# Kernel tuning notes

Measured on AMD Instinct MI355X. Metric: run time of the kernel, lower is better.

## Reference

```python
import jax, jax.numpy as jnp
import numpy as np

DEPTH = 6
N_LEAF = 2 ** DEPTH          # 64
GATE_COUNT = N_LEAF - 1      # 63
IN_F = 512
OUT_F = 512
BATCH = 1024


def setup_inputs() -> dict:
    key = jax.random.key(0)
    k1, k2, k3 = jax.random.split(key, 3)
    x = jax.random.normal(k1, (BATCH, IN_F), dtype=jnp.float32)
    gw = jax.random.normal(k2, (IN_F, GATE_COUNT), dtype=jnp.float32)
    gb = jnp.zeros((GATE_COUNT,), dtype=jnp.float32)
    pw = jax.random.normal(k3, (OUT_F, IN_F, N_LEAF), dtype=jnp.float32)
    pb = jnp.zeros((OUT_F, N_LEAF), dtype=jnp.float32)
    return {"x": x, "gw": gw, "gb": gb, "pw": pw, "pb": pb}


def _leaf_probs(x, gw, gb, depth):
    # gatings: sigmoid(x @ gw + gb), shape [B, gate_count]
    g = jax.nn.sigmoid(x @ gw + gb)
    B = x.shape[0]
    dens = jnp.ones((B, 1), dtype=x.dtype)  # root density
    offset = 0
    for d in range(depth):
        n = 2 ** d
        gp = g[:, offset:offset + n]                    # parent gatings [B, n]
        # left child multiplies by g, right child by (1 - g), interleaved
        pair = jnp.stack([gp, 1.0 - gp], axis=-1).reshape(B, 2 * n)
        dens = jnp.repeat(dens, 2, axis=1) * pair        # [B, 2n]
        offset += n
    return dens  # [B, n_leaf]


def reference(x, gw, gb, pw, pb):
    leaf = _leaf_probs(x, gw, gb, DEPTH)                 # [B, L]
    # per-leaf linear projections, then mix with leaf probabilities
    y = jnp.einsum('bi,oil->bol', x, pw)                 # [B, O, L]
    out = jnp.einsum('bol,bl->bo', y, leaf) + leaf @ pb.T
    return out
```

## Files before the change

### kernel.cpp

```cpp
#include <hip/hip_runtime.h>
#include <hip/hip_bf16.h>

#define TDEPTH 6
#define NLEAF 64
#define NGATE 63
#define INF 512
#define OUTF 512
#define BATCH 1024

#define BM 128
#define BN 64
#define SPLITK 16
#define KCH 513
#define THREADS 256
#define XPITCH 36
#define BPITCH 144

typedef __attribute__((ext_vector_type(4)))  float f32x4;
typedef __attribute__((ext_vector_type(16))) float f32x16;
typedef __attribute__((ext_vector_type(8)))  __bf16 bf16x8;

__global__ __launch_bounds__(256) void leaf_kernel(
    const float* __restrict__ x, const float* __restrict__ gw,
    const float* __restrict__ gb, float* __restrict__ leaf) {
  const int wid = threadIdx.x >> 6, lane = threadIdx.x & 63;
  const int b = blockIdx.x * 4 + wid;
  __shared__ float g[4][NLEAF];
  if (lane < NGATE) {
    const float* xr = x + (size_t)b * INF;
    float a0 = 0.f, a1 = 0.f, a2 = 0.f, a3 = 0.f;
    #pragma unroll 4
    for (int i = 0; i < INF; i += 4) {
      a0 += xr[i + 0] * gw[(i + 0) * NGATE + lane];
      a1 += xr[i + 1] * gw[(i + 1) * NGATE + lane];
      a2 += xr[i + 2] * gw[(i + 2) * NGATE + lane];
      a3 += xr[i + 3] * gw[(i + 3) * NGATE + lane];
    }
    float t = (a0 + a1) + (a2 + a3) + gb[lane];
    g[wid][lane] = 1.0f / (1.0f + __expf(-t));
  }
  __syncthreads();
  float p = 1.0f;
  #pragma unroll
  for (int d = 0; d < TDEPTH; d++) {
    int prefix = lane >> (TDEPTH - 1 - d);
    int node = (1 << d) - 1 + (prefix >> 1);
    float gv = g[wid][node];
    p *= (prefix & 1) ? (1.0f - gv) : gv;
  }
  leaf[(size_t)b * NLEAF + lane] = p;
}

__device__ __forceinline__ void sync_raw() {
  asm volatile("s_waitcnt lgkmcnt(0)" ::: "memory");
  __builtin_amdgcn_sched_barrier(0);
  __builtin_amdgcn_s_barrier();
  __builtin_amdgcn_sched_barrier(0);
}

__global__ __launch_bounds__(THREADS, 4) void gemm_kernel(
    const float* __restrict__ x, const float* __restrict__ pw,
    const float* __restrict__ pb, const float* __restrict__ leaf,
    float* __restrict__ partial) {
  __shared__ __align__(16) float xsm[BM * XPITCH];
  __shared__ __align__(16) __bf16 Bsm[2][BN * (BPITCH/2)];

  const int tid = threadIdx.x;
  const int lane = tid & 63;
  const int wid = tid >> 6;
  const int lo = lane & 31;
  const int half = lane >> 5;

  const int bid = blockIdx.x;
  const int nb = bid & 7, mb = (bid >> 3) & 7, s = bid >> 6;
  const int m0 = mb * BM, n0 = nb * BN;
  const int cs = (s * KCH) / SPLITK;
  const int ce = ((s + 1) * KCH) / SPLITK;
  const int nreal = min(ce, INF) - cs;
  const int total = nreal + ((ce == KCH) ? 1 : 0);

  const int xrow = wid * 32 + lo;

  f32x4 lf[4][2];
  {
    const float* lr = leaf + (size_t)(m0 + xrow) * NLEAF + half * 8;
    #pragma unroll
    for (int t4 = 0; t4 < 4; t4++) {
      lf[t4][0] = *(const f32x4*)(lr + t4 * 16);
      lf[t4][1] = *(const f32x4*)(lr + t4 * 16 + 4);
    }
  }

  {
    int r = tid >> 1, h = tid & 1;
    const float* src = x + (size_t)(m0 + r) * INF + cs + h * 16;
    float* dst = xsm + r * XPITCH + h * 16;
    #pragma unroll
    for (int j = 0; j < 4; j++)
      *(f32x4*)(dst + j * 4) = *(const f32x4*)(src + j * 4);
  }

  const int bo = tid >> 2, bc = tid & 3;
  const float* pwrow = pw + (size_t)(n0 + bo) * (INF * NLEAF) + bc * 16;
  const float* pbrow = pb + (size_t)(n0 + bo) * NLEAF + bc * 16;

  f32x16 acc0 = (f32x16)(0.f), acc1 = (f32x16)(0.f);

  f32x4 bv[4];
  {
    const float* sp = pwrow + (size_t)cs * NLEAF;
    #pragma unroll
    for (int j = 0; j < 4; j++) bv[j] = *(const f32x4*)(sp + j * 4);
    #pragma unroll
    for (int h = 0; h < 2; h++) {
      f32x4 a = bv[2 * h], b = bv[2 * h + 1];
      bf16x8 w;
      w[0] = (__bf16)a[0]; w[1] = (__bf16)a[1];
      w[2] = (__bf16)a[2]; w[3] = (__bf16)a[3];
      w[4] = (__bf16)b[0]; w[5] = (__bf16)b[1];
      w[6] = (__bf16)b[2]; w[7] = (__bf16)b[3];
      *(bf16x8*)((char*)&Bsm[0][0] + bo * BPITCH + bc * 32 + h * 16) = w;
    }
  }
  sync_raw();

  __bf16* cur = &Bsm[0][0];
  __bf16* nxt = &Bsm[1][0];
  for (int t = 0; t < total; ++t) {
    const bool more = (t + 1 < total);
    if (more) {
      const float* sp = (t + 1 < nreal)
          ? pwrow + (size_t)(cs + t + 1) * NLEAF : pbrow;
      #pragma unroll
      for (int j = 0; j < 4; j++) bv[j] = *(const f32x4*)(sp + j * 4);
    }
    float xvr = xsm[xrow * XPITCH + (t & 31)];
    float xv = (t < nreal) ? xvr : 1.0f;
    bf16x8 afr[4];
    #pragma unroll
    for (int t4 = 0; t4 < 4; t4++) {
      f32x4 p0 = lf[t4][0] * xv, p1 = lf[t4][1] * xv;
      bf16x8 a;
      a[0] = (__bf16)p0[0]; a[1] = (__bf16)p0[1];
      a[2] = (__bf16)p0[2]; a[3] = (__bf16)p0[3];
      a[4] = (__bf16)p1[0]; a[5] = (__bf16)p1[1];
      a[6] = (__bf16)p1[2]; a[7] = (__bf16)p1[3];
      afr[t4] = a;
    }
    #pragma unroll
    for (int t4 = 0; t4 < 4; t4++) {
      bf16x8 b0 = *(const bf16x8*)((const char*)cur + lo * BPITCH +
                                   t4 * 32 + half * 16);
      bf16x8 b1 = *(const bf16x8*)((const char*)cur + (32 + lo) * BPITCH +
                                   t4 * 32 + half * 16);
      acc0 = __builtin_amdgcn_mfma_f32_32x32x16_bf16(afr[t4], b0, acc0, 0, 0, 0);
      acc1 = __builtin_amdgcn_mfma_f32_32x32x16_bf16(afr[t4], b1, acc1, 0, 0, 0);
    }
    if (more) {
      #pragma unroll
      for (int h = 0; h < 2; h++) {
        f32x4 a = bv[2 * h], b = bv[2 * h + 1];
        bf16x8 w;
        w[0] = (__bf16)a[0]; w[1] = (__bf16)a[1];
        w[2] = (__bf16)a[2]; w[3] = (__bf16)a[3];
        w[4] = (__bf16)b[0]; w[5] = (__bf16)b[1];
        w[6] = (__bf16)b[2]; w[7] = (__bf16)b[3];
        *(bf16x8*)((char*)nxt + bo * BPITCH + bc * 32 + h * 16) = w;
      }
    }
    sync_raw();
    __bf16* tmp = cur; cur = nxt; nxt = tmp;
  }

  float* dst = partial + ((size_t)s * BATCH + m0 + wid * 32) * OUTF + n0;
  #pragma unroll
  for (int e = 0; e < 16; e++) {
    int row = (e & 3) + 8 * (e >> 2) + 4 * half;
    dst[(size_t)row * OUTF + lo] = acc0[e];
    dst[(size_t)row * OUTF + 32 + lo] = acc1[e];
  }
}

__global__ __launch_bounds__(256) void reduce_kernel(
    const float* __restrict__ partial, float* __restrict__ out) {
  size_t e = ((size_t)blockIdx.x * 256 + threadIdx.x) * 4;
  f32x4 sum = (f32x4){0.f, 0.f, 0.f, 0.f};
  #pragma unroll
  for (int s = 0; s < SPLITK; s++)
    sum += *(const f32x4*)(partial + (size_t)s * BATCH * OUTF + e);
  *(f32x4*)(out + e) = sum;
}

extern "C" void kernel_launch(void* const* d_in, const int* in_sizes, int n_in,
                              void* d_out, int out_size, void* d_ws, size_t ws_size,
                              hipStream_t stream) {
  const float* x  = (const float*)d_in[0];
  const float* gw = (const float*)d_in[1];
  const float* gb = (const float*)d_in[2];
  const float* pw = (const float*)d_in[3];
  const float* pb = (const float*)d_in[4];
  float* out = (float*)d_out;

  float* leaf    = (float*)d_ws;
  float* partial = (float*)((char*)d_ws + (1 << 19));

  leaf_kernel<<<BATCH / 4, 256, 0, stream>>>(x, gw, gb, leaf);
  gemm_kernel<<<(BATCH / BM) * (OUTF / BN) * SPLITK, THREADS, 0, stream>>>(
      x, pw, pb, leaf, partial);
  reduce_kernel<<<(BATCH * OUTF) / (256 * 4), 256, 0, stream>>>(partial, out);
}
```

Before: 74.38 us.

## Load fp32 weights directly into LDS with swizzle and double M tile

The GEMM now stages raw fp32 pw rows into XOR-swizzled LDS using global_load_lds, rather than loading to registers and converting to bf16 before the LDS store. Each wave computes a 64x64 tile with four accumulators (BM raised to 256), so each loaded weight tile serves twice as many rows. Split-K becomes a template parameter, using 32 splits when workspace allows, with a block-index remap to group blocks that share weights. The intent is to cut register-staging overhead and raise weight reuse. In exchange it uses more LDS for fp32 tiles, converts to bf16 on the read side, and writes twice as much partial-sum data for the reduce kernel to read.

```diff
diff --git a/kernel.cpp b/kernel.cpp
--- a/kernel.cpp
+++ b/kernel.cpp
@@ -8,13 +8,10 @@
 #define OUTF 512
 #define BATCH 1024
 
-#define BM 128
+#define BM 256
 #define BN 64
-#define SPLITK 16
+#define THREADS 256
 #define KCH 513
-#define THREADS 256
-#define XPITCH 36
-#define BPITCH 144
 
 typedef __attribute__((ext_vector_type(4)))  float f32x4;
 typedef __attribute__((ext_vector_type(16))) float f32x16;
@@ -51,142 +48,198 @@
   leaf[(size_t)b * NLEAF + lane] = p;
 }
 
-__device__ __forceinline__ void sync_raw() {
-  asm volatile("s_waitcnt lgkmcnt(0)" ::: "memory");
+__device__ __forceinline__ void gload_lds16(const void* g, void* l) {
+  __builtin_amdgcn_global_load_lds(
+      (const __attribute__((address_space(1))) void*)g,
+      (__attribute__((address_space(3))) void*)l, 16, 0, 0);
+}
+
+__device__ __forceinline__ void sync_step() {
   __builtin_amdgcn_sched_barrier(0);
+  asm volatile("s_waitcnt vmcnt(0) lgkmcnt(0)" ::: "memory");
   __builtin_amdgcn_s_barrier();
   __builtin_amdgcn_sched_barrier(0);
 }
 
-__global__ __launch_bounds__(THREADS, 4) void gemm_kernel(
+template <int S>
+__global__ __launch_bounds__(THREADS, 3) void gemm_kernel(
     const float* __restrict__ x, const float* __restrict__ pw,
     const float* __restrict__ pb, const float* __restrict__ leaf,
     float* __restrict__ partial) {
-  __shared__ __align__(16) float xsm[BM * XPITCH];
-  __shared__ __align__(16) __bf16 Bsm[2][BN * (BPITCH/2)];
-
-  const int tid = threadIdx.x;
-  const int lane = tid & 63;
-  const int wid = tid >> 6;
-  const int lo = lane & 31;
-  const int half = lane >> 5;
-
-  const int bid = blockIdx.x;
-  const int nb = bid & 7, mb = (bid >> 3) & 7, s = bid >> 6;
+  constexpr int XN = KCH / S;
+  __shared__ __align__(16) unsigned char Bsm[2][BN * 256];
+  __shared__ __align__(16) float xsm[XN * BM];
+
+  const int tid = threadIdx.x, lane = tid & 63, w = tid >> 6;
+  const int lo = lane & 31, half = lane >> 5;
+
+  constexpr int NWG = 4 * 8 * S;
+  const int L = (blockIdx.x & 7) * (NWG / 8) + (blockIdx.x >> 3);
+  const int mb = L & 3;
+  const int pair = L >> 2;
+  const int nb = pair & 7, s = pair >> 3;
   const int m0 = mb * BM, n0 = nb * BN;
-  const int cs = (s * KCH) / SPLITK;
-  const int ce = ((s + 1) * KCH) / SPLITK;
-  const int nreal = min(ce, INF) - cs;
-  const int total = nreal + ((ce == KCH) ? 1 : 0);
-
-  const int xrow = wid * 32 + lo;
-
-  f32x4 lf[4][2];
+  const int cs = XN * s;
+  const bool bias = (s == S - 1);
+
+  const int lq = lane >> 4;
+  const unsigned cb = (unsigned)(lane & 15) * 16;
+  unsigned pwoff[4];
+  #pragma unroll
+  for (int j = 0; j < 4; j++) {
+    int r = w * 16 + j * 4 + lq;
+    pwoff[j] = (unsigned)(n0 + r) * (unsigned)(INF * NLEAF * 4) +
+               (cb ^ ((unsigned)(r & 7) << 4));
+  }
+  const char* pwc = (const char*)pw;
+  const char* pbc = (const char*)pb;
+
   {
-    const float* lr = leaf + (size_t)(m0 + xrow) * NLEAF + half * 8;
+    const float* src = x + (size_t)(m0 + tid) * INF + cs;
+    float v[XN];
+    #pragma unroll
+    for (int c = 0; c < XN; c += 4) {
+      f32x4 t4v = *(const f32x4*)(src + c);
+      v[c] = t4v[0]; v[c + 1] = t4v[1]; v[c + 2] = t4v[2]; v[c + 3] = t4v[3];
+    }
+    #pragma unroll
+    for (int c = 0; c < XN; c++) xsm[c * BM + tid] = v[c];
+  }
+
+  f32x4 lf[2][4][2];
+  #pragma unroll
+  for (int mr = 0; mr < 2; mr++) {
+    const float* lr = leaf + (size_t)(m0 + w * 64 + mr * 32 + lo) * NLEAF + half * 8;
     #pragma unroll
     for (int t4 = 0; t4 < 4; t4++) {
-      lf[t4][0] = *(const f32x4*)(lr + t4 * 16);
-      lf[t4][1] = *(const f32x4*)(lr + t4 * 16 + 4);
-    }
-  }
-
-  {
-    int r = tid >> 1, h = tid & 1;
-    const float* src = x + (size_t)(m0 + r) * INF + cs + h * 16;
-    float* dst = xsm + r * XPITCH + h * 16;
-    #pragma unroll
-    for (int j = 0; j < 4; j++)
-      *(f32x4*)(dst + j * 4) = *(const f32x4*)(src + j * 4);
-  }
-
-  const int bo = tid >> 2, bc = tid & 3;
-  const float* pwrow = pw + (size_t)(n0 + bo) * (INF * NLEAF) + bc * 16;
-  const float* pbrow = pb + (size_t)(n0 + bo) * NLEAF + bc * 16;
-
-  f32x16 acc0 = (f32x16)(0.f), acc1 = (f32x16)(0.f);
-
-  f32x4 bv[4];
-  {
-    const float* sp = pwrow + (size_t)cs * NLEAF;
-    #pragma unroll
-    for (int j = 0; j < 4; j++) bv[j] = *(const f32x4*)(sp + j * 4);
-    #pragma unroll
-    for (int h = 0; h < 2; h++) {
-      f32x4 a = bv[2 * h], b = bv[2 * h + 1];
-      bf16x8 w;
-      w[0] = (__bf16)a[0]; w[1] = (__bf16)a[1];
-      w[2] = (__bf16)a[2]; w[3] = (__bf16)a[3];
-      w[4] = (__bf16)b[0]; w[5] = (__bf16)b[1];
-      w[6] = (__bf16)b[2]; w[7] = (__bf16)b[3];
-      *(bf16x8*)((char*)&Bsm[0][0] + bo * BPITCH + bc * 32 + h * 16) = w;
-    }
-  }
-  sync_raw();
-
-  __bf16* cur = &Bsm[0][0];
-  __bf16* nxt = &Bsm[1][0];
-  for (int t = 0; t < total; ++t) {
-    const bool more = (t + 1 < total);
-    if (more) {
-      const float* sp = (t + 1 < nreal)
-          ? pwrow + (size_t)(cs + t + 1) * NLEAF : pbrow;
+      lf[mr][t4][0] = *(const f32x4*)(lr + t4 * 16);
+      lf[mr][t4][1] = *(const f32x4*)(lr + t4 * 16 + 4);
+    }
+  }
+
+  auto stage = [&](int buf, int t) {
+    const int i = cs + t;
+    char* dstb = (char*)&Bsm[buf][0] + w * 4096;
+    if (i < INF) {
+      const char* srcb = pwc + (size_t)i * 256;
       #pragma unroll
-      for (int j = 0; j < 4; j++) bv[j] = *(const f32x4*)(sp + j * 4);
-    }
-    float xvr = xsm[xrow * XPITCH + (t & 31)];
-    float xv = (t < nreal) ? xvr : 1.0f;
-    bf16x8 afr[4];
+      for (int j = 0; j < 4; j++) gload_lds16(srcb + pwoff[j], dstb + j * 1024);
+    } else {
+      #pragma unroll
+      for (int j = 0; j < 4; j++) {
+        int r = w * 16 + j * 4 + lq;
+        unsigned o = (unsigned)(n0 + r) * (unsigned)(NLEAF * 4) +
+                     (cb ^ ((unsigned)(r & 7) << 4));
+        gload_lds16(pbc + o, dstb + j * 1024);
+      }
+    }
+  };
+
+  f32x16 acc00 = (f32x16)(0.f), acc01 = (f32x16)(0.f);
+  f32x16 acc10 = (f32x16)(0.f), acc11 = (f32x16)(0.f);
+
+  const unsigned swz = (unsigned)(lo & 7) << 4;
+
+  stage(0, 0);
+  sync_step();
+
+  #pragma unroll 2
+  for (int t = 0; t < XN; t++) {
+    const int cur = t & 1;
+    if (t + 1 < XN || bias) stage(cur ^ 1, t + 1);
+
+    const float xv0 = xsm[t * BM + w * 64 + lo];
+    const float xv1 = xsm[t * BM + w * 64 + 32 + lo];
+    const unsigned char* bufc = &Bsm[cur][0];
+
     #pragma unroll
     for (int t4 = 0; t4 < 4; t4++) {
-      f32x4 p0 = lf[t4][0] * xv, p1 = lf[t4][1] * xv;
-      bf16x8 a;
-      a[0] = (__bf16)p0[0]; a[1] = (__bf16)p0[1];
-      a[2] = (__bf16)p0[2]; a[3] = (__bf16)p0[3];
-      a[4] = (__bf16)p1[0]; a[5] = (__bf16)p1[1];
-      a[6] = (__bf16)p1[2]; a[7] = (__bf16)p1[3];
-      afr[t4] = a;
-    }
+      const unsigned kb = (unsigned)(t4 * 64 + half * 32);
+      f32x4 b0a = *(const f32x4*)(bufc + lo * 256 + ((kb) ^ swz));
+      f32x4 b0b = *(const f32x4*)(bufc + lo * 256 + ((kb + 16) ^ swz));
+      f32x4 b1a = *(const f32x4*)(bufc + (32 + lo) * 256 + ((kb) ^ swz));
+      f32x4 b1b = *(const f32x4*)(bufc + (32 + lo) * 256 + ((kb + 16) ^ swz));
+      bf16x8 bf0, bf1;
+      bf0[0] = (__bf16)b0a[0]; bf0[1] = (__bf16)b0a[1];
+      bf0[2] = (__bf16)b0a[2]; bf0[3] = (__bf16)b0a[3];
+      bf0[4] = (__bf16)b0b[0]; bf0[5] = (__bf16)b0b[1];
+      bf0[6] = (__bf16)b0b[2]; bf0[7] = (__bf16)b0b[3];
+      bf1[0] = (__bf16)b1a[0]; bf1[1] = (__bf16)b1a[1];
+      bf1[2] = (__bf16)b1a[2]; bf1[3] = (__bf16)b1a[3];
+      bf1[4] = (__bf16)b1b[0]; bf1[5] = (__bf16)b1b[1];
+      bf1[6] = (__bf16)b1b[2]; bf1[7] = (__bf16)b1b[3];
+
+      f32x4 p0a = lf[0][t4][0] * xv0, p0b = lf[0][t4][1] * xv0;
+      f32x4 p1a = lf[1][t4][0] * xv1, p1b = lf[1][t4][1] * xv1;
+      bf16x8 a0, a1;
+      a0[0] = (__bf16)p0a[0]; a0[1] = (__bf16)p0a[1];
+      a0[2] = (__bf16)p0a[2]; a0[3] = (__bf16)p0a[3];
+      a0[4] = (__bf16)p0b[0]; a0[5] = (__bf16)p0b[1];
+      a0[6] = (__bf16)p0b[2]; a0[7] = (__bf16)p0b[3];
+      a1[0] = (__bf16)p1a[0]; a1[1] = (__bf16)p1a[1];
+      a1[2] = (__bf16)p1a[2]; a1[3] = (__bf16)p1a[3];
+      a1[4] = (__bf16)p1b[0]; a1[5] = (__bf16)p1b[1];
+      a1[6] = (__bf16)p1b[2]; a1[7] = (__bf16)p1b[3];
+
+      acc00 = __builtin_amdgcn_mfma_f32_32x32x16_bf16(a0, bf0, acc00, 0, 0, 0);
+      acc01 = __builtin_amdgcn_mfma_f32_32x32x16_bf16(a0, bf1, acc01, 0, 0, 0);
+      acc10 = __builtin_amdgcn_mfma_f32_32x32x16_bf16(a1, bf0, acc10, 0, 0, 0);
+      acc11 = __builtin_amdgcn_mfma_f32_32x32x16_bf16(a1, bf1, acc11, 0, 0, 0);
+    }
+    sync_step();
+  }
+
+  if (bias) {
+    const unsigned char* bufc = &Bsm[XN & 1][0];
     #pragma unroll
     for (int t4 = 0; t4 < 4; t4++) {
-      bf16x8 b0 = *(const bf16x8*)((const char*)cur + lo * BPITCH +
-                                   t4 * 32 + half * 16);
-      bf16x8 b1 = *(const bf16x8*)((const char*)cur + (32 + lo) * BPITCH +
-                                   t4 * 32 + half * 16);
-      acc0 = __builtin_amdgcn_mfma_f32_32x32x16_bf16(afr[t4], b0, acc0, 0, 0, 0);
-      acc1 = __builtin_amdgcn_mfma_f32_32x32x16_bf16(afr[t4], b1, acc1, 0, 0, 0);
-    }
-    if (more) {
-      #pragma unroll
-      for (int h = 0; h < 2; h++) {
-        f32x4 a = bv[2 * h], b = bv[2 * h + 1];
-        bf16x8 w;
-        w[0] = (__bf16)a[0]; w[1] = (__bf16)a[1];
-        w[2] = (__bf16)a[2]; w[3] = (__bf16)a[3];
-        w[4] = (__bf16)b[0]; w[5] = (__bf16)b[1];
-        w[6] = (__bf16)b[2]; w[7] = (__bf16)b[3];
-        *(bf16x8*)((char*)nxt + bo * BPITCH + bc * 32 + h * 16) = w;
-      }
-    }
-    sync_raw();
-    __bf16* tmp = cur; cur = nxt; nxt = tmp;
-  }
-
-  float* dst = partial + ((size_t)s * BATCH + m0 + wid * 32) * OUTF + n0;
+      const unsigned kb = (unsigned)(t4 * 64 + half * 32);
+      f32x4 b0a = *(const f32x4*)(bufc + lo * 256 + ((kb) ^ swz));
+      f32x4 b0b = *(const f32x4*)(bufc + lo * 256 + ((kb + 16) ^ swz));
+      f32x4 b1a = *(const f32x4*)(bufc + (32 + lo) * 256 + ((kb) ^ swz));
+      f32x4 b1b = *(const f32x4*)(bufc + (32 + lo) * 256 + ((kb + 16) ^ swz));
+      bf16x8 bf0, bf1, a0, a1;
+      bf0[0] = (__bf16)b0a[0]; bf0[1] = (__bf16)b0a[1];
+      bf0[2] = (__bf16)b0a[2]; bf0[3] = (__bf16)b0a[3];
+      bf0[4] = (__bf16)b0b[0]; bf0[5] = (__bf16)b0b[1];
+      bf0[6] = (__bf16)b0b[2]; bf0[7] = (__bf16)b0b[3];
+      bf1[0] = (__bf16)b1a[0]; bf1[1] = (__bf16)b1a[1];
+      bf1[2] = (__bf16)b1a[2]; bf1[3] = (__bf16)b1a[3];
+      bf1[4] = (__bf16)b1b[0]; bf1[5] = (__bf16)b1b[1];
+      bf1[6] = (__bf16)b1b[2]; bf1[7] = (__bf16)b1b[3];
+      a0[0] = (__bf16)lf[0][t4][0][0]; a0[1] = (__bf16)lf[0][t4][0][1];
+      a0[2] = (__bf16)lf[0][t4][0][2]; a0[3] = (__bf16)lf[0][t4][0][3];
+      a0[4] = (__bf16)lf[0][t4][1][0]; a0[5] = (__bf16)lf[0][t4][1][1];
+      a0[6] = (__bf16)lf[0][t4][1][2]; a0[7] = (__bf16)lf[0][t4][1][3];
+      a1[0] = (__bf16)lf[1][t4][0][0]; a1[1] = (__bf16)lf[1][t4][0][1];
+      a1[2] = (__bf16)lf[1][t4][0][2]; a1[3] = (__bf16)lf[1][t4][0][3];
+      a1[4] = (__bf16)lf[1][t4][1][0]; a1[5] = (__bf16)lf[1][t4][1][1];
+      a1[6] = (__bf16)lf[1][t4][1][2]; a1[7] = (__bf16)lf[1][t4][1][3];
+      acc00 = __builtin_amdgcn_mfma_f32_32x32x16_bf16(a0, bf0, acc00, 0, 0, 0);
+      acc01 = __builtin_amdgcn_mfma_f32_32x32x16_bf16(a0, bf1, acc01, 0, 0, 0);
+      acc10 = __builtin_amdgcn_mfma_f32_32x32x16_bf16(a1, bf0, acc10, 0, 0, 0);
+      acc11 = __builtin_amdgcn_mfma_f32_32x32x16_bf16(a1, bf1, acc11, 0, 0, 0);
+    }
+  }
+
+  float* dst = partial + ((size_t)s * BATCH + m0 + w * 64) * OUTF + n0;
   #pragma unroll
   for (int e = 0; e < 16; e++) {
     int row = (e & 3) + 8 * (e >> 2) + 4 * half;
-    dst[(size_t)row * OUTF + lo] = acc0[e];
-    dst[(size_t)row * OUTF + 32 + lo] = acc1[e];
-  }
-}
-
+    dst[(size_t)row * OUTF + lo] = acc00[e];
+    dst[(size_t)row * OUTF + 32 + lo] = acc01[e];
+    dst[(size_t)(row + 32) * OUTF + lo] = acc10[e];
+    dst[(size_t)(row + 32) * OUTF + 32 + lo] = acc11[e];
+  }
+}
+
+template <int S>
 __global__ __launch_bounds__(256) void reduce_kernel(
     const float* __restrict__ partial, float* __restrict__ out) {
   size_t e = ((size_t)blockIdx.x * 256 + threadIdx.x) * 4;
   f32x4 sum = (f32x4){0.f, 0.f, 0.f, 0.f};
   #pragma unroll
-  for (int s = 0; s < SPLITK; s++)
+  for (int s = 0; s < S; s++)
     sum += *(const f32x4*)(partial + (size_t)s * BATCH * OUTF + e);
   *(f32x4*)(out + e) = sum;
 }
@@ -202,10 +255,16 @@
   float* out = (float*)d_out;
 
   float* leaf    = (float*)d_ws;
-  float* partial = (float*)((char*)d_ws + (1 << 19));
+  float* partial = (float*)((char*)d_ws + (1 << 20));
 
   leaf_kernel<<<BATCH / 4, 256, 0, stream>>>(x, gw, gb, leaf);
-  gemm_kernel<<<(BATCH / BM) * (OUTF / BN) * SPLITK, THREADS, 0, stream>>>(
-      x, pw, pb, leaf, partial);
-  reduce_kernel<<<(BATCH * OUTF) / (256 * 4), 256, 0, stream>>>(partial, out);
-}
+
+  const size_t need32 = (size_t)(1 << 20) + (size_t)32 * BATCH * OUTF * 4;
+  if (ws_size >= need32) {
+    gemm_kernel<32><<<4 * 8 * 32, THREADS, 0, stream>>>(x, pw, pb, leaf, partial);
+    reduce_kernel<32><<<(BATCH * OUTF) / (256 * 4), 256, 0, stream>>>(partial, out);
+  } else {
+    gemm_kernel<16><<<4 * 8 * 16, THREADS, 0, stream>>>(x, pw, pb, leaf, partial);
+    reduce_kernel<16><<<(BATCH * OUTF) / (256 * 4), 256, 0, stream>>>(partial, out);
+  }
+}
```

Result: slower. 108.8 us (+46.2%).

## Pre-convert weights to bf16 MFMA-fragment layout and use single-wave register-fed GEMM blocks

Applied to the files above, without the earlier changes.

A prep kernel, fused with the leaf-probability computation, converts pw and pb to bf16 once per call and stores them in a layout that matches the MFMA B-fragments. The GEMM kernel then reads those fragments straight from global memory into registers with double buffering, which removes the shared-memory staging and the block barriers. Each wave now computes a 128x32 tile with four accumulators, so one B fragment serves four row subtiles. This adds an extra full pass over pw (read fp32, write bf16, read bf16 again) in exchange for cheaper, barrier-free GEMM loops with more reuse per fragment.

```diff
diff --git a/kernel.cpp b/kernel.cpp
--- a/kernel.cpp
+++ b/kernel.cpp
@@ -7,177 +7,167 @@
 #define INF 512
 #define OUTF 512
 #define BATCH 1024
-
-#define BM 128
-#define BN 64
 #define SPLITK 16
-#define KCH 513
-#define THREADS 256
-#define XPITCH 36
-#define BPITCH 144
 
 typedef __attribute__((ext_vector_type(4)))  float f32x4;
 typedef __attribute__((ext_vector_type(16))) float f32x16;
 typedef __attribute__((ext_vector_type(8)))  __bf16 bf16x8;
 
-__global__ __launch_bounds__(256) void leaf_kernel(
+__device__ __forceinline__ bf16x8 pack8(f32x4 a, f32x4 b) {
+  bf16x8 w;
+  w[0] = (__bf16)a[0]; w[1] = (__bf16)a[1];
+  w[2] = (__bf16)a[2]; w[3] = (__bf16)a[3];
+  w[4] = (__bf16)b[0]; w[5] = (__bf16)b[1];
+  w[6] = (__bf16)b[2]; w[7] = (__bf16)b[3];
+  return w;
+}
+
+__global__ __launch_bounds__(256) void prep_kernel(
     const float* __restrict__ x, const float* __restrict__ gw,
-    const float* __restrict__ gb, float* __restrict__ leaf) {
-  const int wid = threadIdx.x >> 6, lane = threadIdx.x & 63;
-  const int b = blockIdx.x * 4 + wid;
-  __shared__ float g[4][NLEAF];
-  if (lane < NGATE) {
-    const float* xr = x + (size_t)b * INF;
-    float a0 = 0.f, a1 = 0.f, a2 = 0.f, a3 = 0.f;
-    #pragma unroll 4
-    for (int i = 0; i < INF; i += 4) {
-      a0 += xr[i + 0] * gw[(i + 0) * NGATE + lane];
-      a1 += xr[i + 1] * gw[(i + 1) * NGATE + lane];
-      a2 += xr[i + 2] * gw[(i + 2) * NGATE + lane];
-      a3 += xr[i + 3] * gw[(i + 3) * NGATE + lane];
-    }
-    float t = (a0 + a1) + (a2 + a3) + gb[lane];
-    g[wid][lane] = 1.0f / (1.0f + __expf(-t));
-  }
-  __syncthreads();
-  float p = 1.0f;
-  #pragma unroll
-  for (int d = 0; d < TDEPTH; d++) {
-    int prefix = lane >> (TDEPTH - 1 - d);
-    int node = (1 << d) - 1 + (prefix >> 1);
-    float gv = g[wid][node];
-    p *= (prefix & 1) ? (1.0f - gv) : gv;
-  }
-  leaf[(size_t)b * NLEAF + lane] = p;
-}
-
-__device__ __forceinline__ void sync_raw() {
-  asm volatile("s_waitcnt lgkmcnt(0)" ::: "memory");
-  __builtin_amdgcn_sched_barrier(0);
-  __builtin_amdgcn_s_barrier();
-  __builtin_amdgcn_sched_barrier(0);
-}
-
-__global__ __launch_bounds__(THREADS, 4) void gemm_kernel(
-    const float* __restrict__ x, const float* __restrict__ pw,
-    const float* __restrict__ pb, const float* __restrict__ leaf,
-    float* __restrict__ partial) {
-  __shared__ __align__(16) float xsm[BM * XPITCH];
-  __shared__ __align__(16) __bf16 Bsm[2][BN * (BPITCH/2)];
-
+    const float* __restrict__ gb, const float* __restrict__ pw,
+    const float* __restrict__ pb, float* __restrict__ leaf,
+    __bf16* __restrict__ pwb) {
   const int tid = threadIdx.x;
-  const int lane = tid & 63;
-  const int wid = tid >> 6;
-  const int lo = lane & 31;
-  const int half = lane >> 5;
-
-  const int bid = blockIdx.x;
-  const int nb = bid & 7, mb = (bid >> 3) & 7, s = bid >> 6;
-  const int m0 = mb * BM, n0 = nb * BN;
-  const int cs = (s * KCH) / SPLITK;
-  const int ce = ((s + 1) * KCH) / SPLITK;
-  const int nreal = min(ce, INF) - cs;
-  const int total = nreal + ((ce == KCH) ? 1 : 0);
-
-  const int xrow = wid * 32 + lo;
-
-  f32x4 lf[4][2];
-  {
-    const float* lr = leaf + (size_t)(m0 + xrow) * NLEAF + half * 8;
+  if (blockIdx.x < 256) {
+    const int wid = tid >> 6, lane = tid & 63;
+    const int b = blockIdx.x * 4 + wid;
+    __shared__ float g[4][NLEAF];
+    if (lane < NGATE) {
+      const float* xr = x + (size_t)b * INF;
+      float a0 = 0.f, a1 = 0.f, a2 = 0.f, a3 = 0.f;
+      #pragma unroll 4
+      for (int i = 0; i < INF; i += 4) {
+        a0 += xr[i + 0] * gw[(i + 0) * NGATE + lane];
+        a1 += xr[i + 1] * gw[(i + 1) * NGATE + lane];
+        a2 += xr[i + 2] * gw[(i + 2) * NGATE + lane];
+        a3 += xr[i + 3] * gw[(i + 3) * NGATE + lane];
+      }
+      float t = (a0 + a1) + (a2 + a3) + gb[lane];
+      g[wid][lane] = 1.0f / (1.0f + __expf(-t));
+    }
+    __syncthreads();
+    float p = 1.0f;
+    #pragma unroll
+    for (int d = 0; d < TDEPTH; d++) {
+      int prefix = lane >> (TDEPTH - 1 - d);
+      int node = (1 << d) - 1 + (prefix >> 1);
+      float gv = g[wid][node];
+      p *= (prefix & 1) ? (1.0f - gv) : gv;
+    }
+    leaf[(size_t)b * NLEAF + lane] = p;
+    return;
+  }
+  const int bid2 = blockIdx.x - 256;
+  const int w = tid >> 6, lane = tid & 63;
+  const int lo = lane & 31, half = lane >> 5;
+  #pragma unroll
+  for (int it = 0; it < 8; it++) {
+    const unsigned S = (unsigned)bid2 * 32 + w * 8 + it;
+    const unsigned i_lin = S >> 2, kc = S & 3;
+    const unsigned nb32 = i_lin / 513;
+    const unsigned i = i_lin - nb32 * 513;
+    const unsigned o = nb32 * 32 + lo;
+    const unsigned l = kc * 16 + half * 8;
+    const float* src = (i < INF) ? (pw + ((size_t)o * INF + i) * NLEAF + l)
+                                 : (pb + (size_t)o * NLEAF + l);
+    f32x4 a = *(const f32x4*)src;
+    f32x4 b = *(const f32x4*)(src + 4);
+    *(bf16x8*)((char*)pwb + (size_t)S * 1024 + (size_t)lane * 16) = pack8(a, b);
+  }
+}
+
+__global__ __launch_bounds__(64, 2) void gemm_kernel(
+    const __bf16* __restrict__ pwb, const float* __restrict__ x,
+    const float* __restrict__ leaf, float* __restrict__ partial) {
+  __shared__ __align__(16) float xsm[32][128];
+
+  const int lane = threadIdx.x;
+  const int lo = lane & 31, half = lane >> 5;
+
+  const int L = ((int)blockIdx.x & 7) * 256 + ((int)blockIdx.x >> 3);
+  const int mb = L & 7;
+  const int rest = L >> 3;
+  const int nb32 = rest & 15, s = rest >> 4;
+  const int m0 = mb * 128, o0 = nb32 * 32;
+  const int cs = s * 32;
+  const int count = 32 + (s == SPLITK - 1 ? 1 : 0);
+
+  #pragma unroll
+  for (int rr = 0; rr < 2; rr++) {
+    const int r = lane + rr * 64;
+    const float* src = x + (size_t)(m0 + r) * INF + cs;
+    #pragma unroll
+    for (int c4 = 0; c4 < 8; c4++) {
+      f32x4 v = *(const f32x4*)(src + c4 * 4);
+      #pragma unroll
+      for (int j = 0; j < 4; j++) xsm[c4 * 4 + j][r] = v[j];
+    }
+  }
+
+  f32x4 lf[4][4][2];
+  #pragma unroll
+  for (int ms = 0; ms < 4; ms++) {
+    const float* lr = leaf + (size_t)(m0 + ms * 32 + lo) * NLEAF + half * 8;
     #pragma unroll
     for (int t4 = 0; t4 < 4; t4++) {
-      lf[t4][0] = *(const f32x4*)(lr + t4 * 16);
-      lf[t4][1] = *(const f32x4*)(lr + t4 * 16 + 4);
-    }
-  }
-
-  {
-    int r = tid >> 1, h = tid & 1;
-    const float* src = x + (size_t)(m0 + r) * INF + cs + h * 16;
-    float* dst = xsm + r * XPITCH + h * 16;
-    #pragma unroll
-    for (int j = 0; j < 4; j++)
-      *(f32x4*)(dst + j * 4) = *(const f32x4*)(src + j * 4);
-  }
-
-  const int bo = tid >> 2, bc = tid & 3;
-  const float* pwrow = pw + (size_t)(n0 + bo) * (INF * NLEAF) + bc * 16;
-  const float* pbrow = pb + (size_t)(n0 + bo) * NLEAF + bc * 16;
-
-  f32x16 acc0 = (f32x16)(0.f), acc1 = (f32x16)(0.f);
-
-  f32x4 bv[4];
-  {
-    const float* sp = pwrow + (size_t)cs * NLEAF;
-    #pragma unroll
-    for (int j = 0; j < 4; j++) bv[j] = *(const f32x4*)(sp + j * 4);
-    #pragma unroll
-    for (int h = 0; h < 2; h++) {
-      f32x4 a = bv[2 * h], b = bv[2 * h + 1];
-      bf16x8 w;
-      w[0] = (__bf16)a[0]; w[1] = (__bf16)a[1];
-      w[2] = (__bf16)a[2]; w[3] = (__bf16)a[3];
-      w[4] = (__bf16)b[0]; w[5] = (__bf16)b[1];
-      w[6] = (__bf16)b[2]; w[7] = (__bf16)b[3];
-      *(bf16x8*)((char*)&Bsm[0][0] + bo * BPITCH + bc * 32 + h * 16) = w;
-    }
-  }
-  sync_raw();
-
-  __bf16* cur = &Bsm[0][0];
-  __bf16* nxt = &Bsm[1][0];
-  for (int t = 0; t < total; ++t) {
-    const bool more = (t + 1 < total);
-    if (more) {
-      const float* sp = (t + 1 < nreal)
-          ? pwrow + (size_t)(cs + t + 1) * NLEAF : pbrow;
+      lf[ms][t4][0] = *(const f32x4*)(lr + t4 * 16);
+      lf[ms][t4][1] = *(const f32x4*)(lr + t4 * 16 + 4);
+    }
+  }
+
+  f32x16 acc[4];
+  #pragma unroll
+  for (int ms = 0; ms < 4; ms++) acc[ms] = (f32x16)(0.f);
+
+  const char* pwt = (const char*)pwb + ((size_t)(nb32 * 513 + cs) << 12) +
+                    (size_t)lane * 16;
+
+  auto loadB = [&](bf16x8(&B)[4], int t) {
+    #pragma unroll
+    for (int f = 0; f < 4; f++)
+      B[f] = *(const bf16x8*)(pwt + ((size_t)t << 12) + (f << 10));
+  };
+
+  auto step = [&](const bf16x8(&B)[4], int t) {
+    const int tx = t & 31;
+    const bool bias = (t >= 32);
+    float xv[4];
+    #pragma unroll
+    for (int ms = 0; ms < 4; ms++)
+      xv[ms] = bias ? 1.0f : xsm[tx][ms * 32 + lo];
+    #pragma unroll
+    for (int t4 = 0; t4 < 4; t4++) {
       #pragma unroll
-      for (int j = 0; j < 4; j++) bv[j] = *(const f32x4*)(sp + j * 4);
-    }
-    float xvr = xsm[xrow * XPITCH + (t & 31)];
-    float xv = (t < nreal) ? xvr : 1.0f;
-    bf16x8 afr[4];
-    #pragma unroll
-    for (int t4 = 0; t4 < 4; t4++) {
-      f32x4 p0 = lf[t4][0] * xv, p1 = lf[t4][1] * xv;
-      bf16x8 a;
-      a[0] = (__bf16)p0[0]; a[1] = (__bf16)p0[1];
-      a[2] = (__bf16)p0[2]; a[3] = (__bf16)p0[3];
-      a[4] = (__bf16)p1[0]; a[5] = (__bf16)p1[1];
-      a[6] = (__bf16)p1[2]; a[7] = (__bf16)p1[3];
-      afr[t4] = a;
-    }
-    #pragma unroll
-    for (int t4 = 0; t4 < 4; t4++) {
-      bf16x8 b0 = *(const bf16x8*)((const char*)cur + lo * BPITCH +
-                                   t4 * 32 + half * 16);
-      bf16x8 b1 = *(const bf16x8*)((const char*)cur + (32 + lo) * BPITCH +
-                                   t4 * 32 + half * 16);
-      acc0 = __builtin_amdgcn_mfma_f32_32x32x16_bf16(afr[t4], b0, acc0, 0, 0, 0);
-      acc1 = __builtin_amdgcn_mfma_f32_32x32x16_bf16(afr[t4], b1, acc1, 0, 0, 0);
-    }
-    if (more) {
-      #pragma unroll
-      for (int h = 0; h < 2; h++) {
-        f32x4 a = bv[2 * h], b = bv[2 * h + 1];
-        bf16x8 w;
-        w[0] = (__bf16)a[0]; w[1] = (__bf16)a[1];
-        w[2] = (__bf16)a[2]; w[3] = (__bf16)a[3];
-        w[4] = (__bf16)b[0]; w[5] = (__bf16)b[1];
-        w[6] = (__bf16)b[2]; w[7] = (__bf16)b[3];
-        *(bf16x8*)((char*)nxt + bo * BPITCH + bc * 32 + h * 16) = w;
+      for (int ms = 0; ms < 4; ms++) {
+        f32x4 pa = lf[ms][t4][0] * xv[ms];
+        f32x4 pc = lf[ms][t4][1] * xv[ms];
+        bf16x8 a = pack8(pa, pc);
+        acc[ms] =
+            __builtin_amdgcn_mfma_f32_32x32x16_bf16(a, B[t4], acc[ms], 0, 0, 0);
       }
     }
-    sync_raw();
-    __bf16* tmp = cur; cur = nxt; nxt = tmp;
-  }
-
-  float* dst = partial + ((size_t)s * BATCH + m0 + wid * 32) * OUTF + n0;
-  #pragma unroll
-  for (int e = 0; e < 16; e++) {
-    int row = (e & 3) + 8 * (e >> 2) + 4 * half;
-    dst[(size_t)row * OUTF + lo] = acc0[e];
-    dst[(size_t)row * OUTF + 32 + lo] = acc1[e];
+  };
+
+  bf16x8 B0[4], B1[4];
+  loadB(B0, 0);
+  int t = 0;
+  while (true) {
+    if (t + 1 < count) loadB(B1, t + 1);
+    step(B0, t);
+    if (++t >= count) break;
+    if (t + 1 < count) loadB(B0, t + 1);
+    step(B1, t);
+    if (++t >= count) break;
+  }
+
+  #pragma unroll
+  for (int ms = 0; ms < 4; ms++) {
+    float* dst = partial + ((size_t)s * BATCH + m0 + ms * 32) * OUTF + o0;
+    #pragma unroll
+    for (int e = 0; e < 16; e++) {
+      int row = (e & 3) + 8 * (e >> 2) + 4 * half;
+      dst[(size_t)row * OUTF + lo] = acc[ms][e];
+    }
   }
 }
 
@@ -201,11 +191,11 @@
   const float* pb = (const float*)d_in[4];
   float* out = (float*)d_out;
 
-  float* leaf    = (float*)d_ws;
-  float* partial = (float*)((char*)d_ws + (1 << 19));
-
-  leaf_kernel<<<BATCH / 4, 256, 0, stream>>>(x, gw, gb, leaf);
-  gemm_kernel<<<(BATCH / BM) * (OUTF / BN) * SPLITK, THREADS, 0, stream>>>(
-      x, pw, pb, leaf, partial);
+  float*  leaf    = (float*)d_ws;
+  __bf16* pwb     = (__bf16*)((char*)d_ws + (256 << 10));
+  float*  partial = (float*)((char*)d_ws + (256 << 10) + (size_t)16 * 513 * 4096);
+
+  prep_kernel<<<256 + 1026, 256, 0, stream>>>(x, gw, gb, pw, pb, leaf, pwb);
+  gemm_kernel<<<2048, 64, 0, stream>>>(pwb, x, leaf, partial);
   reduce_kernel<<<(BATCH * OUTF) / (256 * 4), 256, 0, stream>>>(partial, out);
 }
```

Result: slower. 180.3 us (+142.4%).
